# Optimization experiments

Hardware: AMD Instinct MI355X
Metric: run time of the kernel (lower is better)

## Reference

```python
import jax, jax.numpy as jnp
import numpy as np


def setup_inputs() -> dict:
    key = jax.random.key(0)
    k1, k2 = jax.random.split(key)
    N, K, D = 65536, 512, 512
    x = jax.random.normal(k1, (N, D), dtype=jnp.float32)
    centroids = jax.random.normal(k2, (K, D), dtype=jnp.float32)
    return {"x": x, "centroids": centroids}


def reference(x, centroids):
    # Squared pairwise distances via matmul expansion (same math as
    # sum((x[:,None,:] - c[None,:,:])**2, axis=2), without the [N,K,D] blowup):
    x_sq = jnp.sum(x * x, axis=1, keepdims=True)            # [N, 1]
    c_sq = jnp.sum(centroids * centroids, axis=1)            # [K]
    d2 = x_sq + c_sq[None, :] - 2.0 * (x @ centroids.T)      # [N, K]
    q = 1.0 / (1.0 + d2)                                     # Student-t kernel, alpha=1
    q = q / jnp.sum(q, axis=1, keepdims=True)                # row normalize
    return q
```

## Files before the change

kernel.cpp:

```cpp
#include <hip/hip_runtime.h>
#include <stdint.h>


#define D 512
#define K 512
#define BM 64
#define NKS (D / 32)
#define THREADS 512
#define ESTRIDE 516

typedef __attribute__((ext_vector_type(8))) short short8;
typedef __attribute__((ext_vector_type(4))) float floatx4;

__device__ __forceinline__ uint16_t f2bf(float f) {
  uint32_t u = __float_as_uint(f);
  u += 0x7FFFu + ((u >> 16) & 1u);
  return (uint16_t)(u >> 16);
}

__device__ __forceinline__ uint4 pack8(float4 v0, float4 v1) {
  uint4 pk;
  pk.x = (uint32_t)f2bf(v0.x) | ((uint32_t)f2bf(v0.y) << 16);
  pk.y = (uint32_t)f2bf(v0.z) | ((uint32_t)f2bf(v0.w) << 16);
  pk.z = (uint32_t)f2bf(v1.x) | ((uint32_t)f2bf(v1.y) << 16);
  pk.w = (uint32_t)f2bf(v1.z) | ((uint32_t)f2bf(v1.w) << 16);
  return pk;
}

__device__ __forceinline__ float sq8(float4 v0, float4 v1) {
  return v0.x*v0.x + v0.y*v0.y + v0.z*v0.z + v0.w*v0.w
       + v1.x*v1.x + v1.y*v1.y + v1.z*v1.z + v1.w*v1.w;
}

__global__ __launch_bounds__(64)
void prep_kernel(const float* __restrict__ cent, float* __restrict__ csq,
                 uint16_t* __restrict__ bbf) {
  const int row  = blockIdx.x;
  const int lane = threadIdx.x;
  const float4* src = (const float4*)(cent + (size_t)row * D + lane * 8);
  float4 v0 = src[0];
  float4 v1 = src[1];
  float ss = sq8(v0, v1);
  uint4 pk = pack8(v0, v1);
  const int ks = lane >> 2;
  const int qd = lane & 3;
  const int slot = (ks * 512 + row) * 4 + qd;
  *(uint4*)(bbf + (size_t)slot * 8) = pk;
  #pragma unroll
  for (int m = 1; m < 64; m <<= 1) ss += __shfl_xor(ss, m);
  if (lane == 0) csq[row] = ss;
}

__global__ __launch_bounds__(THREADS, 4)
void cluster_main(const float* __restrict__ x, const uint16_t* __restrict__ bbf,
                  const float* __restrict__ csq, float* __restrict__ out) {
  __shared__ __align__(16) char smem[BM * D * 2];
  __shared__ float lxsq[BM];
  __shared__ float lrow[BM];
  uint16_t* const lA = (uint16_t*)smem;
  float* const ebuf  = (float*)smem;

  const int tid  = threadIdx.x;
  const int wave = tid >> 6;
  const int lane = tid & 63;
  const int p    = lane & 15;
  const int quad = lane >> 4;
  const int row0 = blockIdx.x * BM;

  if (tid < BM) lrow[tid] = 0.f;

  const int ar = tid >> 3;
  const int ag = tid & 7;
  const float* xrow = x + (size_t)(row0 + ar) * D + ag * 8;
  float xacc = 0.f;
  #pragma unroll
  for (int h = 0; h < 2; ++h) {
    float4 v[8];
    #pragma unroll
    for (int j = 0; j < 4; ++j) {
      v[2*j]   = *(const float4*)(xrow + (h*4 + j) * 64);
      v[2*j+1] = *(const float4*)(xrow + (h*4 + j) * 64 + 4);
    }
    #pragma unroll
    for (int j = 0; j < 4; ++j) {
      xacc += sq8(v[2*j], v[2*j+1]);
      const int gi = (h*4 + j) * 8 + ag;
      *(uint4*)(lA + (size_t)ar * 512 + ((gi ^ (ar & 7)) * 8)) =
          pack8(v[2*j], v[2*j+1]);
    }
  }
  xacc += __shfl_xor(xacc, 1);
  xacc += __shfl_xor(xacc, 2);
  xacc += __shfl_xor(xacc, 4);
  if (ag == 0) lxsq[ar] = xacc;

  floatx4 acc[4][4];
  #pragma unroll
  for (int mi = 0; mi < 4; ++mi)
    #pragma unroll
    for (int ni = 0; ni < 4; ++ni)
      acc[mi][ni] = (floatx4){0.f, 0.f, 0.f, 0.f};

  __syncthreads();

  const uint16_t* const bl = bbf + ((wave * 64 + p) * 32 + quad * 8);

  short8 bE[4], bO[4];
  #pragma unroll
  for (int ni = 0; ni < 4; ++ni)
    bE[ni] = *(const short8*)(bl + ni * 512);

  #pragma unroll
  for (int s = 0; s < 8; ++s) {
    const int ks0 = 2 * s, ks1 = 2 * s + 1;

    #pragma unroll
    for (int ni = 0; ni < 4; ++ni)
      bO[ni] = *(const short8*)(bl + ks1 * 16384 + ni * 512);

    #pragma unroll
    for (int mi = 0; mi < 4; ++mi) {
      const int r = mi * 16 + p;
      short8 af = *(const short8*)(
          lA + (size_t)r * 512 + ((((ks0 * 4 + quad) ^ (r & 7))) * 8));
      #pragma unroll
      for (int ni = 0; ni < 4; ++ni)
        acc[mi][ni] = __builtin_amdgcn_mfma_f32_16x16x32_bf16(
            af, bE[ni], acc[mi][ni], 0, 0, 0);
    }

    if (s < 7) {
      #pragma unroll
      for (int ni = 0; ni < 4; ++ni)
        bE[ni] = *(const short8*)(bl + (ks0 + 2) * 16384 + ni * 512);
    }

    #pragma unroll
    for (int mi = 0; mi < 4; ++mi) {
      const int r = mi * 16 + p;
      short8 af = *(const short8*)(
          lA + (size_t)r * 512 + ((((ks1 * 4 + quad) ^ (r & 7))) * 8));
      #pragma unroll
      for (int ni = 0; ni < 4; ++ni)
        acc[mi][ni] = __builtin_amdgcn_mfma_f32_16x16x32_bf16(
            af, bO[ni], acc[mi][ni], 0, 0, 0);
    }
  }

  float xs[4][4];
  #pragma unroll
  for (int mi = 0; mi < 4; ++mi)
    #pragma unroll
    for (int rr = 0; rr < 4; ++rr)
      xs[mi][rr] = lxsq[mi * 16 + quad * 4 + rr];
  float cs[4];
  #pragma unroll
  for (int ni = 0; ni < 4; ++ni)
    cs[ni] = csq[wave * 64 + ni * 16 + p];

  float rp[4][4];
  #pragma unroll
  for (int mi = 0; mi < 4; ++mi)
    #pragma unroll
    for (int rr = 0; rr < 4; ++rr)
      rp[mi][rr] = 0.f;

  #pragma unroll
  for (int mi = 0; mi < 4; ++mi)
    #pragma unroll
    for (int ni = 0; ni < 4; ++ni)
      #pragma unroll
      for (int rr = 0; rr < 4; ++rr) {
        const float d = 1.0f + xs[mi][rr] + cs[ni] - 2.0f * acc[mi][ni][rr];
        const float q = __builtin_amdgcn_rcpf(d);
        acc[mi][ni][rr] = q;
        rp[mi][rr] += q;
      }

  #pragma unroll
  for (int mi = 0; mi < 4; ++mi)
    #pragma unroll
    for (int rr = 0; rr < 4; ++rr) {
      float v = rp[mi][rr];
      v += __shfl_xor(v, 1);
      v += __shfl_xor(v, 2);
      v += __shfl_xor(v, 4);
      v += __shfl_xor(v, 8);
      if (p == 0) atomicAdd(&lrow[mi * 16 + quad * 4 + rr], v);
    }
  __syncthreads();

  float inv[4][4];
  #pragma unroll
  for (int mi = 0; mi < 4; ++mi)
    #pragma unroll
    for (int rr = 0; rr < 4; ++rr)
      inv[mi][rr] = __builtin_amdgcn_rcpf(lrow[mi * 16 + quad * 4 + rr]);

  #pragma unroll
  for (int s = 0; s < 4; ++s) {
    if (s) __syncthreads();
    #pragma unroll
    for (int ni = 0; ni < 4; ++ni)
      #pragma unroll
      for (int rr = 0; rr < 4; ++rr)
        ebuf[(quad * 4 + rr) * ESTRIDE + wave * 64 + ni * 16 + p] =
            acc[s][ni][rr] * inv[s][rr];
    __syncthreads();
    #pragma unroll
    for (int j = 0; j < 4; ++j) {
      const int idx = j * 512 + tid;
      const int r  = idx >> 7;
      const int c4 = idx & 127;
      const float4 v = *(const float4*)&ebuf[r * ESTRIDE + c4 * 4];
      *(float4*)(out + (size_t)(row0 + s * 16 + r) * K + c4 * 4) = v;
    }
  }
}

extern "C" void kernel_launch(void* const* d_in, const int* in_sizes, int n_in,
                              void* d_out, int out_size, void* d_ws, size_t ws_size,
                              hipStream_t stream) {
  const float* x    = (const float*)d_in[0];
  const float* cent = (const float*)d_in[1];
  float* out = (float*)d_out;

  float*    csq = (float*)d_ws;
  uint16_t* bbf = (uint16_t*)((char*)d_ws + 2048);

  const int N = in_sizes[0] / D;
  prep_kernel<<<K, 64, 0, stream>>>(cent, csq, bbf);
  cluster_main<<<N / BM, THREADS, 0, stream>>>(x, bbf, csq, out);
}
```

Measured before the change: 269.0 us.

## Use 1024-thread blocks processing two row tiles with prefetched x loads

Doubles the block to 16 waves, each owning 32 centroid columns instead of 64, and has each block process two 64-row tiles in a loop. The second tile's x rows are loaded into registers during the first tile's epilogue, to hide global load latency. The shared A layout changes to a k-chunked, swizzled arrangement, and syncthreads is replaced by a custom barrier that only waits on LDS counters. The risks are fewer blocks and lower occupancy per CU with 1024 threads, the launch bound of 4 blocks per CU is now likely unattainable, and the lighter barrier could be unsafe around global memory.

Result: slower. 307.2 us (+14.2%).

```diff
diff --git a/kernel.cpp b/kernel.cpp
--- a/kernel.cpp
+++ b/kernel.cpp
@@ -5,12 +5,17 @@
 #define D 512
 #define K 512
 #define BM 64
-#define NKS (D / 32)
-#define THREADS 512
+#define THREADS 1024
 #define ESTRIDE 516
 
 typedef __attribute__((ext_vector_type(8))) short short8;
 typedef __attribute__((ext_vector_type(4))) float floatx4;
+
+#define BARRIER() do {                                      \
+    asm volatile("s_waitcnt lgkmcnt(0)" ::: "memory");      \
+    __builtin_amdgcn_s_barrier();                           \
+    asm volatile("" ::: "memory");                          \
+  } while (0)
 
 __device__ __forceinline__ uint16_t f2bf(float f) {
   uint32_t u = __float_as_uint(f);
@@ -61,159 +66,169 @@
   float* const ebuf  = (float*)smem;
 
   const int tid  = threadIdx.x;
-  const int wave = tid >> 6;
+  const int w    = tid >> 6;
   const int lane = tid & 63;
   const int p    = lane & 15;
   const int quad = lane >> 4;
-  const int row0 = blockIdx.x * BM;
-
-  if (tid < BM) lrow[tid] = 0.f;
-
-  const int ar = tid >> 3;
-  const int ag = tid & 7;
-  const float* xrow = x + (size_t)(row0 + ar) * D + ag * 8;
-  float xacc = 0.f;
-  #pragma unroll
-  for (int h = 0; h < 2; ++h) {
-    float4 v[8];
+  const int ar   = tid >> 4;
+  const int ag   = tid & 15;
+
+  const uint16_t* const bl = bbf + ((w * 32 + p) * 32 + quad * 8);
+
+  const size_t tbase0 = (size_t)blockIdx.x * (2 * BM);
+
+  float4 hv[8];
+  {
+    const float* xr = x + (tbase0 + ar) * D + ag * 8;
     #pragma unroll
     for (int j = 0; j < 4; ++j) {
-      v[2*j]   = *(const float4*)(xrow + (h*4 + j) * 64);
-      v[2*j+1] = *(const float4*)(xrow + (h*4 + j) * 64 + 4);
-    }
+      hv[2*j]   = *(const float4*)(xr + j * 128);
+      hv[2*j+1] = *(const float4*)(xr + j * 128 + 4);
+    }
+  }
+
+  #pragma unroll 1
+  for (int t = 0; t < 2; ++t) {
+    if (t) BARRIER();
+
+    float xacc = 0.f;
     #pragma unroll
     for (int j = 0; j < 4; ++j) {
-      xacc += sq8(v[2*j], v[2*j+1]);
-      const int gi = (h*4 + j) * 8 + ag;
-      *(uint4*)(lA + (size_t)ar * 512 + ((gi ^ (ar & 7)) * 8)) =
-          pack8(v[2*j], v[2*j+1]);
-    }
-  }
-  xacc += __shfl_xor(xacc, 1);
-  xacc += __shfl_xor(xacc, 2);
-  xacc += __shfl_xor(xacc, 4);
-  if (ag == 0) lxsq[ar] = xacc;
-
-  floatx4 acc[4][4];
-  #pragma unroll
-  for (int mi = 0; mi < 4; ++mi)
-    #pragma unroll
-    for (int ni = 0; ni < 4; ++ni)
-      acc[mi][ni] = (floatx4){0.f, 0.f, 0.f, 0.f};
-
-  __syncthreads();
-
-  const uint16_t* const bl = bbf + ((wave * 64 + p) * 32 + quad * 8);
-
-  short8 bE[4], bO[4];
-  #pragma unroll
-  for (int ni = 0; ni < 4; ++ni)
-    bE[ni] = *(const short8*)(bl + ni * 512);
-
-  #pragma unroll
-  for (int s = 0; s < 8; ++s) {
-    const int ks0 = 2 * s, ks1 = 2 * s + 1;
-
-    #pragma unroll
-    for (int ni = 0; ni < 4; ++ni)
-      bO[ni] = *(const short8*)(bl + ks1 * 16384 + ni * 512);
-
+      xacc += sq8(hv[2*j], hv[2*j+1]);
+      const int g = ag + 16 * j;
+      *(uint4*)(lA + (g >> 3) * 4096 + ar * 64 + (((g & 7) ^ (ar & 7)) * 8)) =
+          pack8(hv[2*j], hv[2*j+1]);
+    }
+    xacc += __shfl_xor(xacc, 1);
+    xacc += __shfl_xor(xacc, 2);
+    xacc += __shfl_xor(xacc, 4);
+    xacc += __shfl_xor(xacc, 8);
+    if (ag == 0) lxsq[ar] = xacc;
+    if (tid < BM) lrow[tid] = 0.f;
+    BARRIER();
+
+    floatx4 acc[4][2];
+    #pragma unroll
+    for (int mi = 0; mi < 4; ++mi)
+      #pragma unroll
+      for (int ni = 0; ni < 2; ++ni)
+        acc[mi][ni] = (floatx4){0.f, 0.f, 0.f, 0.f};
+
+    short8 bE[2], bO[2];
+    #pragma unroll
+    for (int ni = 0; ni < 2; ++ni)
+      bE[ni] = *(const short8*)(bl + ni * 512);
+
+    #pragma unroll
+    for (int s8 = 0; s8 < 8; ++s8) {
+      const int ks0 = 2 * s8, ks1 = ks0 + 1;
+
+      #pragma unroll
+      for (int ni = 0; ni < 2; ++ni)
+        bO[ni] = *(const short8*)(bl + ks1 * 16384 + ni * 512);
+
+      #pragma unroll
+      for (int mi = 0; mi < 4; ++mi) {
+        const int r = mi * 16 + p;
+        short8 af = *(const short8*)(
+            lA + (ks0 >> 1) * 4096 + r * 64 +
+            ((((ks0 & 1) * 4 + quad) ^ (r & 7)) * 8));
+        #pragma unroll
+        for (int ni = 0; ni < 2; ++ni)
+          acc[mi][ni] = __builtin_amdgcn_mfma_f32_16x16x32_bf16(
+              af, bE[ni], acc[mi][ni], 0, 0, 0);
+      }
+
+      if (s8 < 7) {
+        #pragma unroll
+        for (int ni = 0; ni < 2; ++ni)
+          bE[ni] = *(const short8*)(bl + (ks0 + 2) * 16384 + ni * 512);
+      }
+
+      #pragma unroll
+      for (int mi = 0; mi < 4; ++mi) {
+        const int r = mi * 16 + p;
+        short8 af = *(const short8*)(
+            lA + (ks1 >> 1) * 4096 + r * 64 +
+            ((((ks1 & 1) * 4 + quad) ^ (r & 7)) * 8));
+        #pragma unroll
+        for (int ni = 0; ni < 2; ++ni)
+          acc[mi][ni] = __builtin_amdgcn_mfma_f32_16x16x32_bf16(
+              af, bO[ni], acc[mi][ni], 0, 0, 0);
+      }
+    }
+
+    if (t == 0) {
+      const float* xr = x + (tbase0 + BM + ar) * D + ag * 8;
+      #pragma unroll
+      for (int j = 0; j < 4; ++j) {
+        hv[2*j]   = *(const float4*)(xr + j * 128);
+        hv[2*j+1] = *(const float4*)(xr + j * 128 + 4);
+      }
+    }
+
+    float cs[2];
+    #pragma unroll
+    for (int ni = 0; ni < 2; ++ni)
+      cs[ni] = csq[w * 32 + ni * 16 + p];
+
+    float rp[4][4];
     #pragma unroll
     for (int mi = 0; mi < 4; ++mi) {
-      const int r = mi * 16 + p;
-      short8 af = *(const short8*)(
-          lA + (size_t)r * 512 + ((((ks0 * 4 + quad) ^ (r & 7))) * 8));
-      #pragma unroll
-      for (int ni = 0; ni < 4; ++ni)
-        acc[mi][ni] = __builtin_amdgcn_mfma_f32_16x16x32_bf16(
-            af, bE[ni], acc[mi][ni], 0, 0, 0);
-    }
-
-    if (s < 7) {
-      #pragma unroll
-      for (int ni = 0; ni < 4; ++ni)
-        bE[ni] = *(const short8*)(bl + (ks0 + 2) * 16384 + ni * 512);
+      #pragma unroll
+      for (int rr = 0; rr < 4; ++rr) rp[mi][rr] = 0.f;
     }
 
     #pragma unroll
     for (int mi = 0; mi < 4; ++mi) {
-      const int r = mi * 16 + p;
-      short8 af = *(const short8*)(
-          lA + (size_t)r * 512 + ((((ks1 * 4 + quad) ^ (r & 7))) * 8));
-      #pragma unroll
-      for (int ni = 0; ni < 4; ++ni)
-        acc[mi][ni] = __builtin_amdgcn_mfma_f32_16x16x32_bf16(
-            af, bO[ni], acc[mi][ni], 0, 0, 0);
-    }
-  }
-
-  float xs[4][4];
-  #pragma unroll
-  for (int mi = 0; mi < 4; ++mi)
-    #pragma unroll
-    for (int rr = 0; rr < 4; ++rr)
-      xs[mi][rr] = lxsq[mi * 16 + quad * 4 + rr];
-  float cs[4];
-  #pragma unroll
-  for (int ni = 0; ni < 4; ++ni)
-    cs[ni] = csq[wave * 64 + ni * 16 + p];
-
-  float rp[4][4];
-  #pragma unroll
-  for (int mi = 0; mi < 4; ++mi)
-    #pragma unroll
-    for (int rr = 0; rr < 4; ++rr)
-      rp[mi][rr] = 0.f;
-
-  #pragma unroll
-  for (int mi = 0; mi < 4; ++mi)
-    #pragma unroll
-    for (int ni = 0; ni < 4; ++ni)
       #pragma unroll
       for (int rr = 0; rr < 4; ++rr) {
-        const float d = 1.0f + xs[mi][rr] + cs[ni] - 2.0f * acc[mi][ni][rr];
-        const float q = __builtin_amdgcn_rcpf(d);
-        acc[mi][ni][rr] = q;
-        rp[mi][rr] += q;
-      }
-
-  #pragma unroll
-  for (int mi = 0; mi < 4; ++mi)
-    #pragma unroll
-    for (int rr = 0; rr < 4; ++rr) {
-      float v = rp[mi][rr];
-      v += __shfl_xor(v, 1);
-      v += __shfl_xor(v, 2);
-      v += __shfl_xor(v, 4);
-      v += __shfl_xor(v, 8);
-      if (p == 0) atomicAdd(&lrow[mi * 16 + quad * 4 + rr], v);
-    }
-  __syncthreads();
-
-  float inv[4][4];
-  #pragma unroll
-  for (int mi = 0; mi < 4; ++mi)
-    #pragma unroll
-    for (int rr = 0; rr < 4; ++rr)
-      inv[mi][rr] = __builtin_amdgcn_rcpf(lrow[mi * 16 + quad * 4 + rr]);
-
-  #pragma unroll
-  for (int s = 0; s < 4; ++s) {
-    if (s) __syncthreads();
-    #pragma unroll
-    for (int ni = 0; ni < 4; ++ni)
+        const float xsv = lxsq[mi * 16 + quad * 4 + rr];
+        #pragma unroll
+        for (int ni = 0; ni < 2; ++ni) {
+          const float d = 1.0f + xsv + cs[ni] - 2.0f * acc[mi][ni][rr];
+          const float q = __builtin_amdgcn_rcpf(d);
+          acc[mi][ni][rr] = q;
+          rp[mi][rr] += q;
+        }
+      }
+    }
+
+    #pragma unroll
+    for (int mi = 0; mi < 4; ++mi)
+      #pragma unroll
+      for (int rr = 0; rr < 4; ++rr) {
+        float v = rp[mi][rr];
+        v += __shfl_xor(v, 1);
+        v += __shfl_xor(v, 2);
+        v += __shfl_xor(v, 4);
+        v += __shfl_xor(v, 8);
+        if (p == 0) atomicAdd(&lrow[mi * 16 + quad * 4 + rr], v);
+      }
+    BARRIER();
+
+    #pragma unroll
+    for (int s = 0; s < 4; ++s) {
+      if (s) BARRIER();
+      float invs[4];
       #pragma unroll
       for (int rr = 0; rr < 4; ++rr)
-        ebuf[(quad * 4 + rr) * ESTRIDE + wave * 64 + ni * 16 + p] =
-            acc[s][ni][rr] * inv[s][rr];
-    __syncthreads();
-    #pragma unroll
-    for (int j = 0; j < 4; ++j) {
-      const int idx = j * 512 + tid;
-      const int r  = idx >> 7;
-      const int c4 = idx & 127;
-      const float4 v = *(const float4*)&ebuf[r * ESTRIDE + c4 * 4];
-      *(float4*)(out + (size_t)(row0 + s * 16 + r) * K + c4 * 4) = v;
+        invs[rr] = __builtin_amdgcn_rcpf(lrow[s * 16 + quad * 4 + rr]);
+      #pragma unroll
+      for (int ni = 0; ni < 2; ++ni)
+        #pragma unroll
+        for (int rr = 0; rr < 4; ++rr)
+          ebuf[(quad * 4 + rr) * ESTRIDE + w * 32 + ni * 16 + p] =
+              acc[s][ni][rr] * invs[rr];
+      BARRIER();
+      #pragma unroll
+      for (int j = 0; j < 2; ++j) {
+        const int idx = j * 1024 + tid;
+        const int r  = idx >> 7;
+        const int c4 = idx & 127;
+        const float4 v = *(const float4*)&ebuf[r * ESTRIDE + c4 * 4];
+        *(float4*)(out + (tbase0 + (size_t)t * BM + s * 16 + r) * K + c4 * 4) = v;
+      }
     }
   }
 }
@@ -230,5 +245,5 @@
 
   const int N = in_sizes[0] / D;
   prep_kernel<<<K, 64, 0, stream>>>(cent, csq, bbf);
-  cluster_main<<<N / BM, THREADS, 0, stream>>>(x, bbf, csq, out);
-}
+  cluster_main<<<N / (2 * BM), THREADS, 0, stream>>>(x, bbf, csq, out);
+}
```
